# Performance work log

Measured on AMD Instinct MI355X. Metric: run time of the kernel, lower is better.

Reference implementation:

```python
import jax, jax.numpy as jnp
import numpy as np

B = 8
T_SCALES = 2
SEQ_LEN = 720
PRED_LEN = 720
ENC_IN = 862
MARK = 4
D_MODEL = 256
N_HEADS = 8
D_FF = 512
D_BLOCK = 720  # == PRED_LEN -> align is Identity
E_LAYERS = 2
EPS = 1e-5


def _ln(x, g, b):
    m = x.mean(-1, keepdims=True)
    v = ((x - m) ** 2).mean(-1, keepdims=True)
    return (x - m) / jnp.sqrt(v + EPS) * g + b


def setup_inputs() -> dict:
    key = jax.random.key(0)
    ks = iter(jax.random.split(key, 64))
    def rn(shape, s=0.02):
        return jax.random.normal(next(ks), shape, jnp.float32) * s
    L, d = E_LAYERS, D_MODEL
    inp = {}
    inp["multi_batch_x"] = jax.random.normal(next(ks), (B, T_SCALES, SEQ_LEN, ENC_IN), jnp.float32)
    inp["multi_batch_x_mark"] = jax.random.normal(next(ks), (B, T_SCALES, SEQ_LEN, MARK), jnp.float32)
    inp["x_dec"] = jnp.zeros((1,), jnp.float32)
    inp["x_mark_dec"] = jnp.zeros((1,), jnp.float32)
    inp["embed_w"] = rn((d, SEQ_LEN)); inp["embed_b"] = jnp.zeros((d,), jnp.float32)
    for nm in ("Wq", "Wk", "Wv", "Wo", "W3", "W4"):
        inp[nm] = rn((L, d, d))
    for nm in ("bq", "bk", "bv", "bo", "b3", "b4"):
        inp[nm] = jnp.zeros((L, d), jnp.float32)
    inp["W1"] = rn((L, D_FF, d)); inp["b1"] = jnp.zeros((L, D_FF), jnp.float32)
    inp["W2"] = rn((L, d, D_FF)); inp["b2"] = jnp.zeros((L, d), jnp.float32)
    inp["W5"] = rn((L, D_BLOCK, 2 * d)); inp["b5"] = jnp.zeros((L, D_BLOCK), jnp.float32)
    inp["W6"] = rn((L, D_BLOCK, 2 * d)); inp["b6"] = jnp.zeros((L, D_BLOCK), jnp.float32)
    inp["ln1_g"] = jnp.ones((L, d), jnp.float32); inp["ln1_b"] = jnp.zeros((L, d), jnp.float32)
    inp["ln2_g"] = jnp.ones((L, d), jnp.float32); inp["ln2_b"] = jnp.zeros((L, d), jnp.float32)
    return inp


def reference(multi_batch_x, multi_batch_x_mark, x_dec, x_mark_dec,
              embed_w, embed_b, Wq, bq, Wk, bk, Wv, bv, Wo, bo,
              W1, b1, W2, b2, W3, b3, W4, b4, W5, b5, W6, b6,
              ln1_g, ln1_b, ln2_g, ln2_b):
    H = N_HEADS
    E = D_MODEL // H
    Bc = multi_batch_x.shape[0]
    scale = 1.0 / jnp.sqrt(jnp.asarray(E, jnp.float32))
    outs = []
    for t in range(T_SCALES):
        x = multi_batch_x[:, t].transpose(0, 2, 1)            # [B, ENC_IN, S]
        mean = x.mean(-1, keepdims=True)
        std = jnp.sqrt(((x - mean) ** 2).mean(-1, keepdims=True) + EPS)
        xn = (x - mean) / std
        xm = multi_batch_x_mark[:, t].transpose(0, 2, 1)      # [B, MARK, S]
        xin = jnp.concatenate([xn, xm], axis=1)               # [B, N, S], N = ENC_IN+MARK
        h = jnp.einsum('bns,ds->bnd', xin, embed_w) + embed_b  # [B, N, d_model]
        N = xin.shape[1]
        output = jnp.zeros((Bc, N, D_BLOCK), h.dtype)
        for l in range(E_LAYERS):
            # full attention (mask_flag=False), dropout in eval mode = identity
            q = (h @ Wq[l].T + bq[l]).reshape(Bc, N, H, E)
            k = (h @ Wk[l].T + bk[l]).reshape(Bc, N, H, E)
            v = (h @ Wv[l].T + bv[l]).reshape(Bc, N, H, E)
            scores = jnp.einsum('blhe,bshe->bhls', q, k) * scale
            A = jax.nn.softmax(scores, axis=-1)
            att = jnp.einsum('bhls,bshd->blhd', A, v).reshape(Bc, N, H * E)
            x_att = att @ Wo[l].T + bo[l]
            x_ln = _ln(h - x_att, ln1_g[l], ln1_b[l])
            # 1x1 conv FFN (conv over channel dim == linear over feature dim)
            y = jax.nn.gelu(x_ln @ W1[l].T + b1[l], approximate=False) @ W2[l].T + b2[l]
            xs = x_ln - y                                      # subtract-residual
            hh = jax.nn.sigmoid(xs @ W3[l].T + b3[l]) * (xs @ W4[l].T + b4[l])
            cat = jnp.concatenate([x_att, y], axis=-1)         # [B, N, 2*d_model]
            out = jax.nn.sigmoid(cat @ W5[l].T + b5[l]) * (cat @ W6[l].T + b6[l])
            h = _ln(hh, ln2_g[l], ln2_b[l])
            output = out - output
        # align = Identity (D_BLOCK == PRED_LEN); keep first ENC_IN channels, invert scaler
        dec = output[:, :ENC_IN, :] * std + mean               # [B, ENC_IN, PRED_LEN]
        outs.append(dec.transpose(0, 2, 1))                    # [B, PRED_LEN, ENC_IN]
    return jnp.stack(outs, axis=-1).mean(axis=-1)
```

## Files before the change

kernel.cpp:

```cpp
#include <hip/hip_runtime.h>
#include <cstdint>
#include <cstddef>

#define DEV __device__ __forceinline__
#define AS1 __attribute__((address_space(1)))
#define AS3 __attribute__((address_space(3)))

typedef unsigned short u16;
typedef unsigned char u8;
typedef long long ll;

typedef __attribute__((ext_vector_type(8))) __bf16 bf16x8;
typedef __attribute__((ext_vector_type(8))) unsigned short u16x8;
typedef __attribute__((ext_vector_type(4))) float f32x4;

static constexpr int SEQ  = 720;
static constexpr int ENC  = 862;
static constexpr int NTOK = 866;
static constexpr int DM   = 256;
static constexpr int G16  = 16;
static constexpr int MTOT = G16 * NTOK;
static constexpr int KPAD = 768;
static constexpr int SPAD = 896;
static constexpr int TCH  = 15;
static constexpr float SC2 = 0.17677669529663689f * 1.4426950408889634f;

DEV float b2f(u16 v){ union { unsigned u; float f; } x; x.u = ((unsigned)v) << 16; return x.f; }
DEV u16 f2b(float f){ union { float f; unsigned u; } x; x.f = f;
  unsigned r = x.u + 0x7fffu + ((x.u >> 16) & 1u); return (u16)(r >> 16); }
DEV bf16x8 as_bf(u16x8 v){ return __builtin_bit_cast(bf16x8, v); }

DEV void g2l(const u16* g, u16* l){
  __builtin_amdgcn_global_load_lds((AS1 void*)g, (AS3 void*)l, 16, 0, 0);
}

DEV int xcd_work(){
  int L = blockIdx.y * gridDim.x + blockIdx.x;
  int T = gridDim.x * gridDim.y;
  int x = L & 7, k = L >> 3;
  int q = T >> 3, r = T & 7;
  int mn = x < r ? x : r;
  return x*q + mn + k;
}

struct CvtJobs {
  const float* src[10];
  u16* dst[10];
  int n[10];
  int per[10];
  ll stride[10];
};
__global__ __launch_bounds__(256) void cvt_multi(CvtJobs J)
{
  int j = blockIdx.y;
  const float* s = J.src[j];
  u16* d = J.dst[j];
  int n = J.n[j], per = J.per[j];
  ll st = J.stride[j];
  for (int i = blockIdx.x*256 + threadIdx.x; i < n; i += gridDim.x*256) {
    ll di = per ? ((ll)(i/per)*st + (i%per)) : (ll)i;
    d[di] = f2b(s[i]);
  }
}

__global__ __launch_bounds__(256) void pack_bqkv(const float* __restrict__ bq,
                                                 const float* __restrict__ bk,
                                                 const float* __restrict__ bv,
                                                 float* __restrict__ out)
{
  int idx = blockIdx.x*256 + threadIdx.x;
  if (idx >= 1536) return;
  int l = idx / 768, j = idx % 768;
  float v;
  if (j < 256)      v = bq[l*256 + j];
  else if (j < 512) v = bk[l*256 + j - 256];
  else              v = bv[l*256 + j - 512];
  out[idx] = v;
}

__global__ __launch_bounds__(256) void stats_part(const float* __restrict__ x,
                                                  float2* __restrict__ part)
{
  int g  = blockIdx.z;
  int tc = blockIdx.y;
  int c  = (blockIdx.x << 8) + threadIdx.x;
  float s = 0.f, q = 0.f;
  if (c < ENC) {
    const float* xp = x + ((ll)g * SEQ + tc * 48) * ENC + c;
    #pragma unroll 8
    for (int t = 0; t < 48; ++t) {
      float v = xp[(ll)t * ENC];
      s += v; q += v * v;
    }
  }
  part[(((ll)g * TCH + tc) * 4 + blockIdx.x) * 256 + threadIdx.x] = make_float2(s, q);
}

__global__ __launch_bounds__(256) void stats_reduce(const float2* __restrict__ part,
                                                    float* __restrict__ meanp,
                                                    float* __restrict__ stdp)
{
  int g  = blockIdx.x >> 2;
  int cc = blockIdx.x & 3;
  int c  = (cc << 8) + threadIdx.x;
  if (c >= ENC) return;
  float s = 0.f, q = 0.f;
  #pragma unroll
  for (int t = 0; t < TCH; ++t) {
    float2 p = part[(((ll)g * TCH + t) * 4 + cc) * 256 + threadIdx.x];
    s += p.x; q += p.y;
  }
  float mn  = s * (1.f / SEQ);
  float var = q * (1.f / SEQ) - mn * mn;
  var = var < 0.f ? 0.f : var;
  meanp[g * ENC + c] = mn;
  stdp [g * ENC + c] = sqrtf(var + 1e-5f);
}

__global__ __launch_bounds__(256) void build_xin(const float* __restrict__ x,
                                                 const float* __restrict__ xm,
                                                 const float* __restrict__ meanp,
                                                 const float* __restrict__ stdp,
                                                 u16* __restrict__ xin)
{
  int g  = blockIdx.z;
  int c0 = blockIdx.x << 5, s0 = blockIdx.y << 5;
  __shared__ float tl[32][33];
  __shared__ float mn[32], isd[32];
  int tid = threadIdx.x;
  if (tid < 32) {
    int c = c0 + tid;
    float m = 0.f, s = 1.f;
    if (c < ENC) { m = meanp[g*ENC + c]; s = stdp[g*ENC + c]; }
    mn[tid] = m; isd[tid] = 1.f / s;
  }
  __syncthreads();
  int ci = tid & 31, r = tid >> 5;
  #pragma unroll
  for (int p = 0; p < 4; ++p) {
    int sl = r + (p << 3);
    int s = s0 + sl, c = c0 + ci;
    float v = 0.f;
    if (s < SEQ && c < NTOK) {
      if (c < ENC) v = (x[((ll)g*SEQ + s)*ENC + c] - mn[ci]) * isd[ci];
      else         v = xm[((ll)g*SEQ + s)*4 + (c - ENC)];
    }
    tl[sl][ci] = v;
  }
  __syncthreads();
  int si = tid & 31;
  #pragma unroll
  for (int p = 0; p < 4; ++p) {
    int cl = r + (p << 3);
    int c = c0 + cl;
    if (c < NTOK) xin[((ll)g*NTOK + c)*KPAD + s0 + si] = f2b(tl[si][cl]);
  }
}

__global__ __launch_bounds__(256) void pack_embedw(const float* __restrict__ ew,
                                                   u16* __restrict__ wp)
{
  int row = blockIdx.x;
  for (int c = threadIdx.x; c < KPAD; c += 256)
    wp[row*KPAD + c] = (c < SEQ) ? f2b(ew[row*SEQ + c]) : (u16)0;
}

__global__ __launch_bounds__(256) void transpose_v(const u16* __restrict__ v, int ldv,
                                                   u16* __restrict__ vT)
{
  int g = blockIdx.z;
  int d0 = blockIdx.x << 5, s0 = blockIdx.y << 5;
  __shared__ u16 tl[32][33];
  int tid = threadIdx.x;
  int di = tid & 31, r = tid >> 5;
  #pragma unroll
  for (int p = 0; p < 4; ++p) {
    int sl = r + (p << 3);
    int s = s0 + sl;
    u16 val = 0;
    if (s < NTOK) val = v[((ll)g*NTOK + s)*ldv + d0 + di];
    tl[sl][di] = val;
  }
  __syncthreads();
  int si = tid & 31;
  #pragma unroll
  for (int p = 0; p < 4; ++p) {
    int dl = r + (p << 3);
    vT[((ll)g*DM + d0 + dl)*SPAD + s0 + si] = tl[si][dl];
  }
}

__global__ __launch_bounds__(256) void flash_attn(const u16* __restrict__ qb,
                                                  const u16* __restrict__ kb,
                                                  int ldqk,
                                                  const u16* __restrict__ vT,
                                                  u16* __restrict__ attb)
{
  const int w = xcd_work();
  const int gh = w / 7;
  const int g = gh >> 3, h = gh & 7;
  const int q0 = (w % 7) * 128;
  const int tid = threadIdx.x, wv = tid >> 6, lane = tid & 63;
  const int q4 = lane >> 4, c16 = lane & 15;
  constexpr int PLD = 136;

  __shared__ __attribute__((aligned(16))) u16 Qs[128*32];
  __shared__ __attribute__((aligned(16))) u16 Ks[128*32];
  __shared__ __attribute__((aligned(16))) u16 Vs[32*PLD];
  __shared__ __attribute__((aligned(16))) u16 Ps[4][32*PLD];

  {
    int r = tid >> 1, sg = (tid & 1) << 4;
    int row = q0 + r; if (row > NTOK-1) row = NTOK-1;
    const u16* src = qb + ((ll)(g*NTOK + row))*ldqk + h*32 + sg;
    *(uint4*)&Qs[r*32 + sg]     = *(const uint4*)src;
    *(uint4*)&Qs[r*32 + sg + 8] = *(const uint4*)(src + 8);
  }
  __syncthreads();

  bf16x8 qf[2];
  qf[0] = as_bf(*(const u16x8*)&Qs[(wv*32 +      c16)*32 + q4*8]);
  qf[1] = as_bf(*(const u16x8*)&Qs[(wv*32 + 16 + c16)*32 + q4*8]);

  float lsum[2][4] = {{0,0,0,0},{0,0,0,0}};
  f32x4 oacc[2][2];
  oacc[0][0] = (f32x4){0,0,0,0}; oacc[0][1] = (f32x4){0,0,0,0};
  oacc[1][0] = (f32x4){0,0,0,0}; oacc[1][1] = (f32x4){0,0,0,0};

  for (int kt = 0; kt < 7; ++kt) {
    const int k0 = kt * 128;
    if (kt) __syncthreads();
    {
      int r = tid >> 1, sg = (tid & 1) << 4;
      int row = k0 + r; if (row > NTOK-1) row = NTOK-1;
      const u16* src = kb + ((ll)(g*NTOK + row))*ldqk + h*32 + sg;
      *(uint4*)&Ks[r*32 + sg]     = *(const uint4*)src;
      *(uint4*)&Ks[r*32 + sg + 8] = *(const uint4*)(src + 8);
    }
    {
      int e = tid >> 3, sg = (tid & 7) << 4;
      const u16* src = vT + ((ll)(g*DM + h*32 + e))*SPAD + k0 + sg;
      *(uint4*)&Vs[e*PLD + sg]     = *(const uint4*)src;
      *(uint4*)&Vs[e*PLD + sg + 8] = *(const uint4*)(src + 8);
    }
    __syncthreads();

    f32x4 s[2][8];
    #pragma unroll
    for (int i = 0; i < 2; ++i)
      #pragma unroll
      for (int j = 0; j < 8; ++j) s[i][j] = (f32x4){0,0,0,0};
    #pragma unroll
    for (int j = 0; j < 8; ++j) {
      bf16x8 kf = as_bf(*(const u16x8*)&Ks[(j*16 + c16)*32 + q4*8]);
      s[0][j] = __builtin_amdgcn_mfma_f32_16x16x32_bf16(qf[0], kf, s[0][j], 0, 0, 0);
      s[1][j] = __builtin_amdgcn_mfma_f32_16x16x32_bf16(qf[1], kf, s[1][j], 0, 0, 0);
    }
    if (kt == 6) {
      #pragma unroll
      for (int j = 0; j < 8; ++j) {
        if (k0 + j*16 + c16 >= NTOK) {
          #pragma unroll
          for (int r = 0; r < 4; ++r) { s[0][j][r] = -1e30f; s[1][j][r] = -1e30f; }
        }
      }
    }

    #pragma unroll
    for (int i = 0; i < 2; ++i)
      #pragma unroll
      for (int j = 0; j < 8; ++j)
        #pragma unroll
        for (int r = 0; r < 4; ++r) {
          float p = exp2f(s[i][j][r]);
          lsum[i][r] += p;
          unsigned u = __builtin_bit_cast(unsigned, p);
          Ps[wv][(i*16 + q4*4 + r)*PLD + j*16 + c16] = (u16)(u >> 16);
        }

    #pragma unroll
    for (int kk = 0; kk < 4; ++kk) {
      bf16x8 af0 = as_bf(*(const u16x8*)&Ps[wv][(     c16)*PLD + kk*32 + q4*8]);
      bf16x8 af1 = as_bf(*(const u16x8*)&Ps[wv][(16 + c16)*PLD + kk*32 + q4*8]);
      bf16x8 b0  = as_bf(*(const u16x8*)&Vs[(     c16)*PLD + kk*32 + q4*8]);
      bf16x8 b1  = as_bf(*(const u16x8*)&Vs[(16 + c16)*PLD + kk*32 + q4*8]);
      oacc[0][0] = __builtin_amdgcn_mfma_f32_16x16x32_bf16(af0, b0, oacc[0][0], 0, 0, 0);
      oacc[0][1] = __builtin_amdgcn_mfma_f32_16x16x32_bf16(af0, b1, oacc[0][1], 0, 0, 0);
      oacc[1][0] = __builtin_amdgcn_mfma_f32_16x16x32_bf16(af1, b0, oacc[1][0], 0, 0, 0);
      oacc[1][1] = __builtin_amdgcn_mfma_f32_16x16x32_bf16(af1, b1, oacc[1][1], 0, 0, 0);
    }
  }

  float linv[2][4];
  #pragma unroll
  for (int i = 0; i < 2; ++i)
    #pragma unroll
    for (int r = 0; r < 4; ++r) {
      float t = lsum[i][r];
      t += __shfl_xor(t, 1, 64);
      t += __shfl_xor(t, 2, 64);
      t += __shfl_xor(t, 4, 64);
      t += __shfl_xor(t, 8, 64);
      linv[i][r] = 1.f / t;
    }
  #pragma unroll
  for (int i = 0; i < 2; ++i)
    #pragma unroll
    for (int jn = 0; jn < 2; ++jn)
      #pragma unroll
      for (int r = 0; r < 4; ++r) {
        int row = q0 + wv*32 + i*16 + q4*4 + r;
        if (row < NTOK)
          attb[((ll)(g*NTOK + row))*DM + h*32 + jn*16 + c16] =
            f2b(oacc[i][jn][r] * linv[i][r]);
      }
}

__global__ __launch_bounds__(256) void ln_rows(const u16* __restrict__ in1,
                                               const u16* __restrict__ in2,
                                               int ld1, int ld2,
                                               const float* __restrict__ gamma,
                                               const float* __restrict__ beta,
                                               u16* __restrict__ out, int ldo, int Mrows)
{
  int row = blockIdx.x*4 + (threadIdx.x >> 6);
  int lane = threadIdx.x & 63;
  if (row >= Mrows) return;
  float xv[4];
  ushort4 a = *(const ushort4*)(in1 + (ll)row*ld1 + lane*4);
  xv[0]=b2f(a.x); xv[1]=b2f(a.y); xv[2]=b2f(a.z); xv[3]=b2f(a.w);
  if (in2) {
    ushort4 b = *(const ushort4*)(in2 + (ll)row*ld2 + lane*4);
    xv[0]-=b2f(b.x); xv[1]-=b2f(b.y); xv[2]-=b2f(b.z); xv[3]-=b2f(b.w);
  }
  float s = xv[0]+xv[1]+xv[2]+xv[3];
  #pragma unroll
  for (int o = 32; o > 0; o >>= 1) s += __shfl_xor(s, o, 64);
  float mean = s * (1.f/256.f);
  float d0=xv[0]-mean, d1=xv[1]-mean, d2=xv[2]-mean, d3=xv[3]-mean;
  float q = d0*d0 + d1*d1 + d2*d2 + d3*d3;
  #pragma unroll
  for (int o = 32; o > 0; o >>= 1) q += __shfl_xor(q, o, 64);
  float rstd = 1.f / sqrtf(q * (1.f/256.f) + 1e-5f);
  float4 gv = *(const float4*)(gamma + lane*4);
  float4 bb = *(const float4*)(beta  + lane*4);
  ushort4 o4;
  o4.x = f2b(d0*rstd*gv.x + bb.x);
  o4.y = f2b(d1*rstd*gv.y + bb.y);
  o4.z = f2b(d2*rstd*gv.z + bb.z);
  o4.w = f2b(d3*rstd*gv.w + bb.w);
  *(ushort4*)(out + (ll)row*ldo + lane*4) = o4;
}

__global__ __launch_bounds__(256) void final_combine(const u16* __restrict__ outF,
                                                     const float* __restrict__ meanp,
                                                     const float* __restrict__ stdp,
                                                     float* __restrict__ dout)
{
  int b = blockIdx.z;
  int c0 = blockIdx.x << 5, s0 = blockIdx.y << 5;
  __shared__ float tl[32][33];
  int tid = threadIdx.x;
  int si = tid & 31, r = tid >> 5;
  #pragma unroll
  for (int p = 0; p < 4; ++p) {
    int cl = r + (p << 3);
    int c = c0 + cl, s = s0 + si;
    float accv = 0.f;
    #pragma unroll
    for (int t = 0; t < 2; ++t) {
      int g = b*2 + t;
      if (c < ENC && s < SEQ) {
        float v = b2f(outF[((ll)(g*NTOK + c))*SEQ + s]);
        accv += 0.5f * (v * stdp[g*ENC + c] + meanp[g*ENC + c]);
      }
    }
    tl[cl][si] = accv;
  }
  __syncthreads();
  int ci = tid & 31;
  #pragma unroll
  for (int p = 0; p < 4; ++p) {
    int sl = r + (p << 3);
    int s = s0 + sl, c = c0 + ci;
    if (s < SEQ && c < ENC)
      dout[((ll)b*SEQ + s)*ENC + c] = tl[ci][sl];
  }
}

template<int NB>
__global__ __launch_bounds__(256, NB == 1 ? 5 : 3) void gemm64(
    const u16* __restrict__ A, const u16* __restrict__ B0, const u16* __restrict__ B1,
    const float* __restrict__ bias0, const float* __restrict__ bias1,
    u16* __restrict__ C,
    const u16* __restrict__ aux1, u16* __restrict__ aux2, const u16* __restrict__ sub,
    int M, int N, int K, int lda, int ldb, int ldc, int ld1, int ld2, int ldsub, int mode)
{
  __shared__ __attribute__((aligned(16))) u16 S[8192 * (1 + NB)];

  const int tid  = threadIdx.x;
  const int wv   = tid >> 6;
  const int lane = tid & 63;
  const int q4   = lane >> 4;
  const int c16  = lane & 15;

  const int w  = xcd_work();
  const int n0 = (w % gridDim.x) * 64;
  const int m0 = (w / gridDim.x) * 64;
  const int wm = (wv >> 1) * 32;
  const int wn = (wv & 1) * 32;

  const int lrow = lane >> 2;
  const int lcol = (((lane & 3) ^ ((lrow >> 1) & 3)) << 3);

  int arow = m0 + wv*16 + lrow; if (arow >= M) arow = M-1;
  int brow = n0 + wv*16 + lrow; if (brow >= N) brow = N-1;
  const u16* pa  = A  + (ll)arow*lda + lcol;
  const u16* pb0 = B0 + (ll)brow*ldb + lcol;
  const u16* pb1 = (NB == 2) ? B1 + (ll)brow*ldb + lcol : nullptr;

  f32x4 acc0[2][2];
  f32x4 acc1[2][2];
  #pragma unroll
  for (int i = 0; i < 2; ++i)
    #pragma unroll
    for (int j = 0; j < 2; ++j) {
      acc0[i][j] = (f32x4){0,0,0,0};
      if constexpr (NB == 2) acc1[i][j] = (f32x4){0,0,0,0};
    }

  const int nk = K >> 6;
  auto issue = [&](int kt2, int p) {
    const int ko = kt2 * 64;
    #pragma unroll
    for (int c = 0; c < 2; ++c) {
      g2l(pa  + ko + c*32, &S[(p*2 + c)*2048 + (wv*16)*32]);
      g2l(pb0 + ko + c*32, &S[8192 + (p*2 + c)*2048 + (wv*16)*32]);
      if constexpr (NB == 2)
        g2l(pb1 + ko + c*32, &S[16384 + (p*2 + c)*2048 + (wv*16)*32]);
    }
  };

  issue(0, 0);
  for (int kt = 0; kt < nk; ++kt) {
    const int p = kt & 1;
    if (kt + 1 < nk) {
      issue(kt + 1, p ^ 1);
      if constexpr (NB == 1) asm volatile("s_waitcnt vmcnt(4)" ::: "memory");
      else                   asm volatile("s_waitcnt vmcnt(6)" ::: "memory");
    } else {
      asm volatile("s_waitcnt vmcnt(0)" ::: "memory");
    }
    __builtin_amdgcn_s_barrier();
    asm volatile("" ::: "memory");

    const int sw = ((q4 ^ ((c16 >> 1) & 3)) << 3);
    #pragma unroll
    for (int c = 0; c < 2; ++c) {
      const u16* as_ = &S[(p*2 + c)*2048];
      const u16* b0s = &S[8192 + (p*2 + c)*2048];
      bf16x8 af[2], bfv[2];
      #pragma unroll
      for (int i = 0; i < 2; ++i)
        af[i] = as_bf(*(const u16x8*)&as_[(wm + i*16 + c16)*32 + sw]);
      #pragma unroll
      for (int j = 0; j < 2; ++j)
        bfv[j] = as_bf(*(const u16x8*)&b0s[(wn + j*16 + c16)*32 + sw]);
      #pragma unroll
      for (int i = 0; i < 2; ++i)
        #pragma unroll
        for (int j = 0; j < 2; ++j)
          acc0[i][j] = __builtin_amdgcn_mfma_f32_16x16x32_bf16(af[i], bfv[j], acc0[i][j], 0, 0, 0);
      if constexpr (NB == 2) {
        const u16* b1s = &S[16384 + (p*2 + c)*2048];
        bf16x8 b1v[2];
        #pragma unroll
        for (int j = 0; j < 2; ++j)
          b1v[j] = as_bf(*(const u16x8*)&b1s[(wn + j*16 + c16)*32 + sw]);
        #pragma unroll
        for (int i = 0; i < 2; ++i)
          #pragma unroll
          for (int j = 0; j < 2; ++j)
            acc1[i][j] = __builtin_amdgcn_mfma_f32_16x16x32_bf16(af[i], b1v[j], acc1[i][j], 0, 0, 0);
      }
    }

    asm volatile("s_waitcnt lgkmcnt(0)" ::: "memory");
    __builtin_amdgcn_s_barrier();
  }

  #pragma unroll
  for (int i = 0; i < 2; ++i) {
    #pragma unroll
    for (int j = 0; j < 2; ++j) {
      int n = n0 + wn + j*16 + c16;
      if (n >= N) continue;
      float bv0 = bias0 ? bias0[n] : 0.f;
      float bv1 = (NB == 2) ? bias1[n] : 0.f;
      int mb = m0 + wm + i*16 + q4*4;
      #pragma unroll
      for (int r = 0; r < 4; ++r) {
        int m = mb + r;
        if (m >= M) continue;
        ll ci = (ll)m*ldc + n;
        if constexpr (NB == 2) {
          float z5 = acc0[i][j][r] + bv0;
          float z6 = acc1[i][j][r] + bv1;
          float v = z6 / (1.f + expf(-z5));
          if (sub) v -= b2f(sub[(ll)m*ldsub + n]);
          C[ci] = f2b(v);
        } else {
          float x = acc0[i][j][r] + bv0;
          if (mode == 0) {
            C[ci] = f2b(x);
          } else if (mode == 1) {
            C[ci] = f2b(0.5f * x * (1.f + erff(x * 0.70710678118654752f)));
          } else if (mode == 5) {
            C[ci] = f2b(n < 256 ? x * SC2 : x);
          } else {
            C[ci] = f2b(x);
            float xl = b2f(aux1[(ll)m*ld1 + n]);
            aux2[(ll)m*ld2 + n] = f2b(xl - x);
          }
        }
      }
    }
  }
}

__global__ __launch_bounds__(256, 4) void gemm128d(
    const u16* __restrict__ A, const u16* __restrict__ B0, const u16* __restrict__ B1,
    const float* __restrict__ bias0, const float* __restrict__ bias1,
    u16* __restrict__ C, const u16* __restrict__ sub,
    int M, int N, int K, int lda, int ldb, int ldc, int ldsub)
{
  __shared__ __attribute__((aligned(16))) u16 S[16384];

  const int tid  = threadIdx.x;
  const int wv   = tid >> 6;
  const int lane = tid & 63;
  const int q4   = lane >> 4;
  const int c16  = lane & 15;

  const int w  = xcd_work();
  const int n0 = (w % gridDim.x) * 64;
  const int m0 = (w / gridDim.x) * 128;
  const int wm = (wv >> 1) * 64;
  const int wn = (wv & 1) * 32;

  const int lrow = lane >> 2;
  const int lcol = (((lane & 3) ^ ((lrow >> 1) & 3)) << 3);

  int ar0 = m0 + wv*32 + lrow;      if (ar0 >= M) ar0 = M-1;
  int ar1 = m0 + wv*32 + 16 + lrow; if (ar1 >= M) ar1 = M-1;
  int br  = n0 + wv*16 + lrow;      if (br  >= N) br  = N-1;
  const u16* pa0 = A  + (ll)ar0*lda + lcol;
  const u16* pa1 = A  + (ll)ar1*lda + lcol;
  const u16* pb0 = B0 + (ll)br*ldb + lcol;
  const u16* pb1 = B1 + (ll)br*ldb + lcol;

  f32x4 acc0[4][2], acc1[4][2];
  #pragma unroll
  for (int i = 0; i < 4; ++i)
    #pragma unroll
    for (int j = 0; j < 2; ++j) {
      acc0[i][j] = (f32x4){0,0,0,0};
      acc1[i][j] = (f32x4){0,0,0,0};
    }

  const int nk = K >> 5;
  auto issue = [&](int kt2, int p) {
    const int ko = kt2 * 32;
    g2l(pa0 + ko, &S[p*4096 + (wv*32)*32]);
    g2l(pa1 + ko, &S[p*4096 + (wv*32 + 16)*32]);
    g2l(pb0 + ko, &S[8192  + p*2048 + (wv*16)*32]);
    g2l(pb1 + ko, &S[12288 + p*2048 + (wv*16)*32]);
  };

  issue(0, 0);
  for (int kt = 0; kt < nk; ++kt) {
    const int p = kt & 1;
    if (kt + 1 < nk) {
      issue(kt + 1, p ^ 1);
      asm volatile("s_waitcnt vmcnt(4)" ::: "memory");
    } else {
      asm volatile("s_waitcnt vmcnt(0)" ::: "memory");
    }
    __builtin_amdgcn_s_barrier();
    asm volatile("" ::: "memory");

    const int sw = ((q4 ^ ((c16 >> 1) & 3)) << 3);
    const u16* as_ = &S[p*4096];
    const u16* b0s = &S[8192  + p*2048];
    const u16* b1s = &S[12288 + p*2048];
    bf16x8 af[4], b0v[2], b1v[2];
    #pragma unroll
    for (int i = 0; i < 4; ++i)
      af[i] = as_bf(*(const u16x8*)&as_[(wm + i*16 + c16)*32 + sw]);
    #pragma unroll
    for (int j = 0; j < 2; ++j) {
      b0v[j] = as_bf(*(const u16x8*)&b0s[(wn + j*16 + c16)*32 + sw]);
      b1v[j] = as_bf(*(const u16x8*)&b1s[(wn + j*16 + c16)*32 + sw]);
    }
    #pragma unroll
    for (int i = 0; i < 4; ++i)
      #pragma unroll
      for (int j = 0; j < 2; ++j) {
        acc0[i][j] = __builtin_amdgcn_mfma_f32_16x16x32_bf16(af[i], b0v[j], acc0[i][j], 0, 0, 0);
        acc1[i][j] = __builtin_amdgcn_mfma_f32_16x16x32_bf16(af[i], b1v[j], acc1[i][j], 0, 0, 0);
      }

    asm volatile("s_waitcnt lgkmcnt(0)" ::: "memory");
    __builtin_amdgcn_s_barrier();
  }

  #pragma unroll
  for (int i = 0; i < 4; ++i) {
    #pragma unroll
    for (int j = 0; j < 2; ++j) {
      int n = n0 + wn + j*16 + c16;
      if (n >= N) continue;
      float bv0 = bias0[n], bv1 = bias1[n];
      int mb = m0 + wm + i*16 + q4*4;
      #pragma unroll
      for (int r = 0; r < 4; ++r) {
        int m = mb + r;
        if (m >= M) continue;
        float z5 = acc0[i][j][r] + bv0;
        float z6 = acc1[i][j][r] + bv1;
        float v = z6 / (1.f + expf(-z5));
        if (sub) v -= b2f(sub[(ll)m*ldsub + n]);
        C[(ll)m*ldc + n] = f2b(v);
      }
    }
  }
}

extern "C" void kernel_launch(void* const* d_in, const int* in_sizes, int n_in,
                              void* d_out, int out_size, void* d_ws, size_t ws_size,
                              hipStream_t stream)
{
  (void)in_sizes; (void)n_in; (void)out_size; (void)ws_size;
  const float* x    = (const float*)d_in[0];
  const float* xm   = (const float*)d_in[1];
  const float* embw = (const float*)d_in[4];
  const float* embb = (const float*)d_in[5];
  const float* Wqf  = (const float*)d_in[6];
  const float* Wkf  = (const float*)d_in[7];
  const float* Wvf  = (const float*)d_in[8];
  const float* Wof  = (const float*)d_in[9];
  const float* W3f  = (const float*)d_in[10];
  const float* W4f  = (const float*)d_in[11];
  const float* bq   = (const float*)d_in[12];
  const float* bk   = (const float*)d_in[13];
  const float* bv   = (const float*)d_in[14];
  const float* bo   = (const float*)d_in[15];
  const float* b3   = (const float*)d_in[16];
  const float* b4   = (const float*)d_in[17];
  const float* W1f  = (const float*)d_in[18];
  const float* b1   = (const float*)d_in[19];
  const float* W2f  = (const float*)d_in[20];
  const float* b2   = (const float*)d_in[21];
  const float* W5f  = (const float*)d_in[22];
  const float* b5   = (const float*)d_in[23];
  const float* W6f  = (const float*)d_in[24];
  const float* b6   = (const float*)d_in[25];
  const float* ln1g = (const float*)d_in[26];
  const float* ln1b = (const float*)d_in[27];
  const float* ln2g = (const float*)d_in[28];
  const float* ln2b = (const float*)d_in[29];

  u8* ws = (u8*)d_ws;
  size_t off = 0;
  auto alloc = [&](size_t bytes) -> void* {
    void* ptr = ws + off;
    off = (off + bytes + 255) & ~(size_t)255;
    return ptr;
  };
  float* meanp = (float*)alloc((size_t)G16*ENC*4);
  float* stdp  = (float*)alloc((size_t)G16*ENC*4);
  float* partp = (float*)alloc((size_t)G16*TCH*1024*2*4);
  u16* xin   = (u16*)alloc((size_t)G16*NTOK*KPAD*2);
  u16* wp    = (u16*)alloc((size_t)DM*KPAD*2);
  const int nWsm = 2*DM*DM;
  const int nWff = 2*512*DM;
  const int nW56 = 2*SEQ*512;
  u16* Wqkv = (u16*)alloc((size_t)2*768*256*2);
  u16* Wo = (u16*)alloc((size_t)nWsm*2);
  u16* W3 = (u16*)alloc((size_t)nWsm*2);
  u16* W4 = (u16*)alloc((size_t)nWsm*2);
  u16* W1 = (u16*)alloc((size_t)nWff*2);
  u16* W2 = (u16*)alloc((size_t)nWff*2);
  u16* W5 = (u16*)alloc((size_t)nW56*2);
  u16* W6 = (u16*)alloc((size_t)nW56*2);
  float* bqkv = (float*)alloc((size_t)2*768*4);
  u16* hb    = (u16*)alloc((size_t)MTOT*DM*2);
  u16* qkvb  = (u16*)alloc((size_t)MTOT*768*2);
  u16* vT    = (u16*)alloc((size_t)G16*DM*SPAD*2);
  u16* attb  = (u16*)alloc((size_t)MTOT*DM*2);
  u16* catb  = (u16*)alloc((size_t)MTOT*512*2);
  u16* xlnb  = (u16*)alloc((size_t)MTOT*DM*2);
  u16* t1b   = (u16*)alloc((size_t)MTOT*512*2);
  u16* xsb   = (u16*)alloc((size_t)MTOT*DM*2);
  u16* hhb   = (u16*)alloc((size_t)MTOT*DM*2);
  u16* out0b = (u16*)alloc((size_t)MTOT*SEQ*2);
  u16* outFb = (u16*)alloc((size_t)MTOT*SEQ*2);

  auto gemm64_1 = [&](const u16* A, int lda, const u16* B, int ldb, const float* bias,
                      u16* C, int ldc, int M, int N, int K, int mode,
                      const u16* a1, int ld1, u16* a2, int ld2) {
    dim3 grid((N + 63) / 64, (M + 63) / 64, 1);
    gemm64<1><<<grid, 256, 0, stream>>>(A, B, nullptr, bias, nullptr, C, a1, a2, nullptr,
                                        M, N, K, lda, ldb, ldc, ld1, ld2, 0, mode);
  };
  auto gemm64_2 = [&](const u16* A, int lda, const u16* B0p, const u16* B1p, int ldb,
                      const float* bias0, const float* bias1, u16* C, int ldc,
                      const u16* sub, int ldsub, int M, int N, int K) {
    dim3 grid((N + 63) / 64, (M + 63) / 64, 1);
    gemm64<2><<<grid, 256, 0, stream>>>(A, B0p, B1p, bias0, bias1, C, nullptr, nullptr, sub,
                                        M, N, K, lda, ldb, ldc, 0, 0, ldsub, 0);
  };
  auto gemmD128 = [&](const u16* A, int lda, const u16* B0p, const u16* B1p, int ldb,
                      const float* bias0, const float* bias1, u16* C, int ldc,
                      const u16* sub, int ldsub, int M, int N, int K) {
    dim3 grid((N + 63) / 64, (M + 127) / 128, 1);
    gemm128d<<<grid, 256, 0, stream>>>(A, B0p, B1p, bias0, bias1, C, sub,
                                       M, N, K, lda, ldb, ldc, ldsub);
  };

  CvtJobs J{};
  int nj = 0;
  auto addjob = [&](const float* s, u16* d, int n, int per, ll stride) {
    J.src[nj] = s; J.dst[nj] = d; J.n[nj] = n; J.per[nj] = per; J.stride[nj] = stride; nj++;
  };
  addjob(Wqf, Wqkv,           nWsm, 65536, 196608);
  addjob(Wkf, Wqkv + 65536,   nWsm, 65536, 196608);
  addjob(Wvf, Wqkv + 131072,  nWsm, 65536, 196608);
  addjob(Wof, Wo, nWsm, 0, 0);
  addjob(W3f, W3, nWsm, 0, 0);
  addjob(W4f, W4, nWsm, 0, 0);
  addjob(W1f, W1, nWff, 0, 0);
  addjob(W2f, W2, nWff, 0, 0);
  addjob(W5f, W5, nW56, 0, 0);
  addjob(W6f, W6, nW56, 0, 0);
  cvt_multi<<<dim3(512, 10), 256, 0, stream>>>(J);
  pack_bqkv<<<6, 256, 0, stream>>>(bq, bk, bv, bqkv);

  stats_part<<<dim3(4, TCH, 16), 256, 0, stream>>>(x, (float2*)partp);
  stats_reduce<<<64, 256, 0, stream>>>((const float2*)partp, meanp, stdp);
  build_xin<<<dim3(28, 24, 16), 256, 0, stream>>>(x, xm, meanp, stdp, xin);
  pack_embedw<<<256, 256, 0, stream>>>(embw, wp);

  gemm64_1(xin, KPAD, wp, KPAD, embb, hb, DM, MTOT, DM, KPAD, 0, nullptr, 0, nullptr, 0);

  for (int l = 0; l < 2; ++l) {
    const ll wOff = (ll)l * DM * DM;
    gemm64_1(hb, DM, Wqkv + (ll)l*768*256, 256, bqkv + l*768, qkvb, 768,
             MTOT, 768, DM, 5, nullptr, 0, nullptr, 0);
    transpose_v<<<dim3(8, 28, 16), 256, 0, stream>>>(qkvb + 512, 768, vT);

    flash_attn<<<dim3(7, 128), 256, 0, stream>>>(qkvb, qkvb + 256, 768, vT, attb);

    gemm64_1(attb, DM, Wo + wOff, DM, bo + l*DM, catb, 512, MTOT, DM, DM, 0, nullptr, 0, nullptr, 0);
    ln_rows<<<MTOT/4, 256, 0, stream>>>(hb, catb, DM, 512, ln1g + l*DM, ln1b + l*DM, xlnb, DM, MTOT);
    gemm64_1(xlnb, DM, W1 + (ll)l*512*DM, DM, b1 + l*512, t1b, 512, MTOT, 512, DM, 1, nullptr, 0, nullptr, 0);
    gemm64_1(t1b, 512, W2 + (ll)l*DM*512, 512, b2 + l*DM, catb + 256, 512, MTOT, DM, 512, 2, xlnb, DM, xsb, DM);
    gemm64_2(xsb, DM, W3 + wOff, W4 + wOff, DM, b3 + l*DM, b4 + l*DM, hhb, DM,
             nullptr, 0, MTOT, DM, DM);
    ln_rows<<<MTOT/4, 256, 0, stream>>>(hhb, nullptr, DM, 0, ln2g + l*DM, ln2b + l*DM, hb, DM, MTOT);
    if (l == 0)
      gemmD128(catb, 512, W5 + (ll)l*SEQ*512, W6 + (ll)l*SEQ*512, 512,
               b5 + l*SEQ, b6 + l*SEQ, out0b, SEQ, nullptr, 0, MTOT, SEQ, 512);
    else
      gemmD128(catb, 512, W5 + (ll)l*SEQ*512, W6 + (ll)l*SEQ*512, 512,
               b5 + l*SEQ, b6 + l*SEQ, outFb, SEQ, out0b, SEQ, MTOT, SEQ, 512);
  }

  final_combine<<<dim3(27, 23, 8), 256, 0, stream>>>(outFb, meanp, stdp, (float*)d_out);
}
```

Before: 602.8 us.

## Replace LDS-staged dual GEMM with register-direct loads and smaller tiles

The gated W5/W6 dual GEMM no longer stages tiles through shared memory with async global-to-LDS copies and barriers. Each lane now loads its MFMA fragments straight from global memory into registers, double-buffered in registers, and the M tile shrinks from 128 to 64 rows. This removes LDS traffic and barrier stalls, and the launch bound changes from 4 to 3 blocks per SM to fit the extra registers. The cost is that tiles are no longer shared inside a block, so global and L2 traffic rises, and loads of 16 bytes per lane along K may coalesce poorly.

```diff
diff --git a/kernel.cpp b/kernel.cpp
--- a/kernel.cpp
+++ b/kernel.cpp
@@ -528,14 +528,12 @@
   }
 }
 
-__global__ __launch_bounds__(256, 4) void gemm128d(
+__global__ __launch_bounds__(256, 3) void gemm_reg_dual(
     const u16* __restrict__ A, const u16* __restrict__ B0, const u16* __restrict__ B1,
     const float* __restrict__ bias0, const float* __restrict__ bias1,
     u16* __restrict__ C, const u16* __restrict__ sub,
     int M, int N, int K, int lda, int ldb, int ldc, int ldsub)
 {
-  __shared__ __attribute__((aligned(16))) u16 S[16384];
-
   const int tid  = threadIdx.x;
   const int wv   = tid >> 6;
   const int lane = tid & 63;
@@ -544,78 +542,72 @@
 
   const int w  = xcd_work();
   const int n0 = (w % gridDim.x) * 64;
-  const int m0 = (w / gridDim.x) * 128;
-  const int wm = (wv >> 1) * 64;
+  const int m0 = (w / gridDim.x) * 64;
+  const int wm = (wv >> 1) * 32;
   const int wn = (wv & 1) * 32;
 
-  const int lrow = lane >> 2;
-  const int lcol = (((lane & 3) ^ ((lrow >> 1) & 3)) << 3);
-
-  int ar0 = m0 + wv*32 + lrow;      if (ar0 >= M) ar0 = M-1;
-  int ar1 = m0 + wv*32 + 16 + lrow; if (ar1 >= M) ar1 = M-1;
-  int br  = n0 + wv*16 + lrow;      if (br  >= N) br  = N-1;
-  const u16* pa0 = A  + (ll)ar0*lda + lcol;
-  const u16* pa1 = A  + (ll)ar1*lda + lcol;
-  const u16* pb0 = B0 + (ll)br*ldb + lcol;
-  const u16* pb1 = B1 + (ll)br*ldb + lcol;
-
-  f32x4 acc0[4][2], acc1[4][2];
-  #pragma unroll
-  for (int i = 0; i < 4; ++i)
+  int ar0 = m0 + wm + c16;      if (ar0 >= M) ar0 = M-1;
+  int ar1 = m0 + wm + 16 + c16; if (ar1 >= M) ar1 = M-1;
+  int br0 = n0 + wn + c16;      if (br0 >= N) br0 = N-1;
+  int br1 = n0 + wn + 16 + c16; if (br1 >= N) br1 = N-1;
+  const u16* pa0 = A  + (ll)ar0*lda + q4*8;
+  const u16* pa1 = A  + (ll)ar1*lda + q4*8;
+  const u16* p00 = B0 + (ll)br0*ldb + q4*8;
+  const u16* p01 = B0 + (ll)br1*ldb + q4*8;
+  const u16* p10 = B1 + (ll)br0*ldb + q4*8;
+  const u16* p11 = B1 + (ll)br1*ldb + q4*8;
+
+  f32x4 acc0[2][2], acc1[2][2];
+  #pragma unroll
+  for (int i = 0; i < 2; ++i)
     #pragma unroll
     for (int j = 0; j < 2; ++j) {
       acc0[i][j] = (f32x4){0,0,0,0};
       acc1[i][j] = (f32x4){0,0,0,0};
     }
 
-  const int nk = K >> 5;
-  auto issue = [&](int kt2, int p) {
-    const int ko = kt2 * 32;
-    g2l(pa0 + ko, &S[p*4096 + (wv*32)*32]);
-    g2l(pa1 + ko, &S[p*4096 + (wv*32 + 16)*32]);
-    g2l(pb0 + ko, &S[8192  + p*2048 + (wv*16)*32]);
-    g2l(pb1 + ko, &S[12288 + p*2048 + (wv*16)*32]);
+  u16x8 a_[2][2], x_[2][2], y_[2][2];
+  u16x8 an[2][2], xn[2][2], yn[2][2];
+  auto load_all = [&](u16x8 (&aa)[2][2], u16x8 (&xx)[2][2], u16x8 (&yy)[2][2], int k0) {
+    #pragma unroll
+    for (int c = 0; c < 2; ++c) {
+      const int o = k0 + c*32;
+      aa[c][0] = *(const u16x8*)(pa0 + o);
+      aa[c][1] = *(const u16x8*)(pa1 + o);
+      xx[c][0] = *(const u16x8*)(p00 + o);
+      xx[c][1] = *(const u16x8*)(p01 + o);
+      yy[c][0] = *(const u16x8*)(p10 + o);
+      yy[c][1] = *(const u16x8*)(p11 + o);
+    }
   };
 
-  issue(0, 0);
+  const int nk = K >> 6;
+  load_all(a_, x_, y_, 0);
   for (int kt = 0; kt < nk; ++kt) {
-    const int p = kt & 1;
-    if (kt + 1 < nk) {
-      issue(kt + 1, p ^ 1);
-      asm volatile("s_waitcnt vmcnt(4)" ::: "memory");
-    } else {
-      asm volatile("s_waitcnt vmcnt(0)" ::: "memory");
-    }
-    __builtin_amdgcn_s_barrier();
-    asm volatile("" ::: "memory");
-
-    const int sw = ((q4 ^ ((c16 >> 1) & 3)) << 3);
-    const u16* as_ = &S[p*4096];
-    const u16* b0s = &S[8192  + p*2048];
-    const u16* b1s = &S[12288 + p*2048];
-    bf16x8 af[4], b0v[2], b1v[2];
-    #pragma unroll
-    for (int i = 0; i < 4; ++i)
-      af[i] = as_bf(*(const u16x8*)&as_[(wm + i*16 + c16)*32 + sw]);
-    #pragma unroll
-    for (int j = 0; j < 2; ++j) {
-      b0v[j] = as_bf(*(const u16x8*)&b0s[(wn + j*16 + c16)*32 + sw]);
-      b1v[j] = as_bf(*(const u16x8*)&b1s[(wn + j*16 + c16)*32 + sw]);
-    }
-    #pragma unroll
-    for (int i = 0; i < 4; ++i)
-      #pragma unroll
-      for (int j = 0; j < 2; ++j) {
-        acc0[i][j] = __builtin_amdgcn_mfma_f32_16x16x32_bf16(af[i], b0v[j], acc0[i][j], 0, 0, 0);
-        acc1[i][j] = __builtin_amdgcn_mfma_f32_16x16x32_bf16(af[i], b1v[j], acc1[i][j], 0, 0, 0);
+    const int k1 = (kt + 1 < nk) ? (kt + 1) * 64 : 0;
+    load_all(an, xn, yn, k1);
+    #pragma unroll
+    for (int c = 0; c < 2; ++c) {
+      #pragma unroll
+      for (int i = 0; i < 2; ++i)
+        #pragma unroll
+        for (int j = 0; j < 2; ++j) {
+          acc0[i][j] = __builtin_amdgcn_mfma_f32_16x16x32_bf16(as_bf(a_[c][i]), as_bf(x_[c][j]), acc0[i][j], 0, 0, 0);
+          acc1[i][j] = __builtin_amdgcn_mfma_f32_16x16x32_bf16(as_bf(a_[c][i]), as_bf(y_[c][j]), acc1[i][j], 0, 0, 0);
+        }
+    }
+    #pragma unroll
+    for (int c = 0; c < 2; ++c)
+      #pragma unroll
+      for (int u = 0; u < 2; ++u) {
+        a_[c][u] = an[c][u];
+        x_[c][u] = xn[c][u];
+        y_[c][u] = yn[c][u];
       }
-
-    asm volatile("s_waitcnt lgkmcnt(0)" ::: "memory");
-    __builtin_amdgcn_s_barrier();
-  }
-
-  #pragma unroll
-  for (int i = 0; i < 4; ++i) {
+  }
+
+  #pragma unroll
+  for (int i = 0; i < 2; ++i) {
     #pragma unroll
     for (int j = 0; j < 2; ++j) {
       int n = n0 + wn + j*16 + c16;
@@ -720,12 +712,12 @@
     gemm64<2><<<grid, 256, 0, stream>>>(A, B0p, B1p, bias0, bias1, C, nullptr, nullptr, sub,
                                         M, N, K, lda, ldb, ldc, 0, 0, ldsub, 0);
   };
-  auto gemmD128 = [&](const u16* A, int lda, const u16* B0p, const u16* B1p, int ldb,
+  auto gemmDreg = [&](const u16* A, int lda, const u16* B0p, const u16* B1p, int ldb,
                       const float* bias0, const float* bias1, u16* C, int ldc,
                       const u16* sub, int ldsub, int M, int N, int K) {
-    dim3 grid((N + 63) / 64, (M + 127) / 128, 1);
-    gemm128d<<<grid, 256, 0, stream>>>(A, B0p, B1p, bias0, bias1, C, sub,
-                                       M, N, K, lda, ldb, ldc, ldsub);
+    dim3 grid((N + 63) / 64, (M + 63) / 64, 1);
+    gemm_reg_dual<<<grid, 256, 0, stream>>>(A, B0p, B1p, bias0, bias1, C, sub,
+                                            M, N, K, lda, ldb, ldc, ldsub);
   };
 
   CvtJobs J{};
@@ -769,10 +761,10 @@
              nullptr, 0, MTOT, DM, DM);
     ln_rows<<<MTOT/4, 256, 0, stream>>>(hhb, nullptr, DM, 0, ln2g + l*DM, ln2b + l*DM, hb, DM, MTOT);
     if (l == 0)
-      gemmD128(catb, 512, W5 + (ll)l*SEQ*512, W6 + (ll)l*SEQ*512, 512,
+      gemmDreg(catb, 512, W5 + (ll)l*SEQ*512, W6 + (ll)l*SEQ*512, 512,
                b5 + l*SEQ, b6 + l*SEQ, out0b, SEQ, nullptr, 0, MTOT, SEQ, 512);
     else
-      gemmD128(catb, 512, W5 + (ll)l*SEQ*512, W6 + (ll)l*SEQ*512, 512,
+      gemmDreg(catb, 512, W5 + (ll)l*SEQ*512, W6 + (ll)l*SEQ*512, 512,
                b5 + l*SEQ, b6 + l*SEQ, outFb, SEQ, out0b, SEQ, MTOT, SEQ, 512);
   }
 
```

Result: slower. 759.4 us (+26.0%).
